# Kernel tuning notes

Measured on AMD Instinct MI355X. Metric: run time of the kernel, lower is better.

## Reference

```python
import jax, jax.numpy as jnp
import numpy as np

LN_EPS = 1e-7

def gelu(x):
    # BERT erf-based gelu
    return 0.5 * x * (1.0 + jax.lax.erf(x / jnp.sqrt(2.0).astype(x.dtype)))

def setup_inputs() -> dict:
    key = jax.random.key(0)
    k1, k2 = jax.random.split(key)
    B, S, H, I = 4, 4096, 1024, 4096
    hidden_states = jax.random.normal(k1, (B, S, H), dtype=jnp.float32)
    W = jax.random.normal(k2, (H, I), dtype=jnp.float32) * (1.0 / np.sqrt(H))
    b = jnp.zeros((I,), dtype=jnp.float32)
    ln_gamma = jnp.ones((H,), dtype=jnp.float32)
    ln_beta = jnp.zeros((H,), dtype=jnp.float32)
    return {"hidden_states": hidden_states, "ln_gamma": ln_gamma, "ln_beta": ln_beta, "W": W, "b": b}

def reference(hidden_states, ln_gamma, ln_beta, W, b):
    # LayerNorm over last dim
    mu = jnp.mean(hidden_states, axis=-1, keepdims=True)
    xc = hidden_states - mu
    var = jnp.mean(xc * xc, axis=-1, keepdims=True)
    x_norm = xc * jax.lax.rsqrt(var + LN_EPS) * ln_gamma + ln_beta
    # Linear projection [B,S,H] @ [H,I] + b, then gelu
    y = jnp.einsum('bsh,hi->bsi', x_norm, W) + b
    return gelu(y)
```

## Files before the change

kernel.cpp:

```cpp
#include <hip/hip_runtime.h>
#include <hip/hip_bf16.h>

typedef __attribute__((ext_vector_type(8))) short bf16x8;
typedef __attribute__((ext_vector_type(4))) float f32x4;

static __device__ __forceinline__ unsigned short f2bf(float f) {
    unsigned u = __builtin_bit_cast(unsigned, f);
    unsigned rounding = 0x7fffu + ((u >> 16) & 1u);
    u += rounding;
    return (unsigned short)(u >> 16);
}

static __device__ __forceinline__ void async_copy16(const void* g, void* l) {
    __builtin_amdgcn_global_load_lds(
        (const __attribute__((address_space(1))) unsigned int*)g,
        (__attribute__((address_space(3))) unsigned int*)l,
        16, 0, 0);
}

#define BARRIER() __builtin_amdgcn_s_barrier()
#define VM0()    do { asm volatile("s_waitcnt vmcnt(0)" ::: "memory"); \
                      __builtin_amdgcn_sched_barrier(0); } while (0)

static __device__ __forceinline__ float fast_gelu(float y) {
    float u = 0.7978845608028654f * y * (1.0f + 0.044715f * y * y);
    float au = fminf(fabsf(u), 9.0f);
    float e = __expf(-2.0f * au);
    float th = (1.0f - e) * __builtin_amdgcn_rcpf(1.0f + e);
    th = (u < 0.0f) ? -th : th;
    return 0.5f * y * (1.0f + th);
}

__global__ __launch_bounds__(256) void ln_cast_kernel(
    const float* __restrict__ x, const float* __restrict__ gamma,
    const float* __restrict__ beta, unsigned short* __restrict__ out) {
    const int row = blockIdx.x;
    const int t = threadIdx.x;
    const float4 v = ((const float4*)(x + (size_t)row * 1024))[t];

    float s  = v.x + v.y + v.z + v.w;
    float ss = v.x * v.x + v.y * v.y + v.z * v.z + v.w * v.w;
    #pragma unroll
    for (int off = 32; off; off >>= 1) {
        s  += __shfl_down(s, off);
        ss += __shfl_down(ss, off);
    }
    __shared__ float red[8];
    const int wid = t >> 6, lane = t & 63;
    if (lane == 0) { red[wid] = s; red[wid + 4] = ss; }
    __syncthreads();
    if (t == 0) {
        float S  = red[0] + red[1] + red[2] + red[3];
        float SS = red[4] + red[5] + red[6] + red[7];
        float mu = S * (1.0f / 1024.0f);
        float var = SS * (1.0f / 1024.0f) - mu * mu;
        red[0] = mu;
        red[1] = rsqrtf(var + 1e-7f);
    }
    __syncthreads();
    const float mu = red[0], rs = red[1];
    const float4 g = ((const float4*)gamma)[t];
    const float4 b = ((const float4*)beta)[t];

    ushort4 pk;
    pk.x = f2bf((v.x - mu) * rs * g.x + b.x);
    pk.y = f2bf((v.y - mu) * rs * g.y + b.y);
    pk.z = f2bf((v.z - mu) * rs * g.z + b.z);
    pk.w = f2bf((v.w - mu) * rs * g.w + b.w);
    ((ushort4*)(out + (size_t)row * 1024))[t] = pk;
}

__global__ __launch_bounds__(256) void wt_cast_kernel(
    const float* __restrict__ W, unsigned short* __restrict__ Wt) {
    __shared__ float tile[32][33];
    const int bx = blockIdx.x;
    const int by = blockIdx.y;
    const int tx = threadIdx.x & 31;
    const int ty = threadIdx.x >> 5;
    #pragma unroll
    for (int i = 0; i < 4; ++i) {
        int k = by * 32 + ty + i * 8;
        tile[ty + i * 8][tx] = W[(size_t)k * 4096 + bx * 32 + tx];
    }
    __syncthreads();
    #pragma unroll
    for (int i = 0; i < 4; ++i) {
        int n = bx * 32 + ty + i * 8;
        Wt[(size_t)n * 1024 + by * 32 + tx] = f2bf(tile[tx][ty + i * 8]);
    }
}

__global__ __launch_bounds__(512, 2) void gemm_kernel(
    const unsigned short* __restrict__ A, const unsigned short* __restrict__ Wt,
    const float* __restrict__ bias, float* __restrict__ out) {
    __shared__ char lds_mem[131072];

    const int bid = blockIdx.x;
    const int swz = (bid & 7) * 128 + (bid >> 3);
    const int bm = swz >> 4;
    const int bn = swz & 15;

    const int t = threadIdx.x;
    const int lane = t & 63;
    const int wid = t >> 6;
    const int wm = wid >> 2;
    const int wn = wid & 3;
    const int lrow = lane & 15;
    const int lk = lane >> 4;

    const int srr = t >> 3;
    const int sch = t & 7;
    const int sgc = sch ^ (srr & 7);
    const unsigned short* gA = A  + (size_t)(bm * 256 + srr) * 1024 + sgc * 8;
    const unsigned short* gB = Wt + (size_t)(bn * 256 + srr) * 1024 + sgc * 8;
    const int lst = srr * 128 + sch * 16;

    auto stage = [&](int kt, char* buf) {
        #pragma unroll
        for (int i = 0; i < 4; ++i) {
            async_copy16(gA + (size_t)(i * 64) * 1024 + kt * 64, buf + i * 64 * 128 + lst);
            async_copy16(gB + (size_t)(i * 64) * 1024 + kt * 64, buf + 32768 + i * 64 * 128 + lst);
        }
    };

    const int ck0 = ((lk) ^ (lrow & 7)) * 16;
    const int ck1 = ((4 + lk) ^ (lrow & 7)) * 16;
    const int aBase = (wm * 128 + lrow) * 128;
    const int bBase = 32768 + (wn * 64 + lrow) * 128;

    f32x4 acc[8][4];
    #pragma unroll
    for (int i = 0; i < 8; ++i)
        #pragma unroll
        for (int j = 0; j < 4; ++j) acc[i][j] = (f32x4)0.0f;

    float bv[4];
    #pragma unroll
    for (int ni = 0; ni < 4; ++ni) bv[ni] = bias[bn * 256 + wn * 64 + ni * 16 + lrow];

    stage(0, lds_mem);
    VM0();
    BARRIER();

    const int NKT = 16;
    for (int kt = 0; kt < NKT; ++kt) {
        char* cbuf = lds_mem + ((kt & 1) << 16);
        char* nbuf = lds_mem + (((kt + 1) & 1) << 16);

        bf16x8 bf[4][2];
        #pragma unroll
        for (int ni = 0; ni < 4; ++ni) {
            const char* p = cbuf + bBase + ni * 16 * 128;
            bf[ni][0] = *(const bf16x8*)(p + ck0);
            bf[ni][1] = *(const bf16x8*)(p + ck1);
        }

        if (kt + 1 < NKT) stage(kt + 1, nbuf);

        __builtin_amdgcn_s_setprio(1);
        #pragma unroll
        for (int mi = 0; mi < 8; ++mi) {
            const char* p = cbuf + aBase + mi * 16 * 128;
            bf16x8 a0 = *(const bf16x8*)(p + ck0);
            bf16x8 a1 = *(const bf16x8*)(p + ck1);
            #pragma unroll
            for (int ni = 0; ni < 4; ++ni) {
                acc[mi][ni] = __builtin_amdgcn_mfma_f32_16x16x32_bf16(a0, bf[ni][0], acc[mi][ni], 0, 0, 0);
                acc[mi][ni] = __builtin_amdgcn_mfma_f32_16x16x32_bf16(a1, bf[ni][1], acc[mi][ni], 0, 0, 0);
            }
        }
        __builtin_amdgcn_s_setprio(0);

        if (kt + 1 < NKT) {
            VM0();
            BARRIER();
        }
    }

    #pragma unroll
    for (int mi = 0; mi < 8; ++mi) {
        const int row0 = bm * 256 + wm * 128 + mi * 16 + lk * 4;
        #pragma unroll
        for (int ni = 0; ni < 4; ++ni) {
            const int col = bn * 256 + wn * 64 + ni * 16 + lrow;
            #pragma unroll
            for (int r = 0; r < 4; ++r) {
                float y = acc[mi][ni][r] + bv[ni];
                out[(size_t)(row0 + r) * 4096 + col] = fast_gelu(y);
            }
        }
    }
}

extern "C" void kernel_launch(void* const* d_in, const int* in_sizes, int n_in,
                              void* d_out, int out_size, void* d_ws, size_t ws_size,
                              hipStream_t stream) {
    const float* hidden = (const float*)d_in[0];
    const float* gamma  = (const float*)d_in[1];
    const float* beta   = (const float*)d_in[2];
    const float* W      = (const float*)d_in[3];
    const float* bias   = (const float*)d_in[4];
    float* out = (float*)d_out;

    unsigned short* Abf = (unsigned short*)d_ws;
    unsigned short* Wt  = (unsigned short*)((char*)d_ws + (size_t)16384 * 1024 * 2);

    ln_cast_kernel<<<16384, 256, 0, stream>>>(hidden, gamma, beta, Abf);
    wt_cast_kernel<<<dim3(128, 32), 256, 0, stream>>>(W, Wt);
    gemm_kernel<<<1024, 512, 0, stream>>>(Abf, Wt, bias, out);
}
```

Measured before the change: 184.6 us.

## Triple-buffer GEMM LDS with prefetch distance two and smaller K tile

The GEMM K-tile is halved from 64 to 32, so it now takes 32 iterations. LDS goes from two 64 KB buffers to three 32 KB buffers, with loads issued two tiles ahead and a partial vmcnt wait, so global loads are no longer fully drained before each barrier. The LDS swizzle and load mapping are rewritten for 64-byte rows. The trade-off is twice as many barriers and fewer MFMAs between them, in exchange for deeper latency hiding and a smaller LDS footprint.

```diff
diff --git a/kernel.cpp b/kernel.cpp
--- a/kernel.cpp
+++ b/kernel.cpp
@@ -19,7 +19,7 @@
 }
 
 #define BARRIER() __builtin_amdgcn_s_barrier()
-#define VM0()    do { asm volatile("s_waitcnt vmcnt(0)" ::: "memory"); \
+#define VMCNT(N) do { asm volatile("s_waitcnt vmcnt(" #N ")" ::: "memory"); \
                       __builtin_amdgcn_sched_barrier(0); } while (0)
 
 static __device__ __forceinline__ float fast_gelu(float y) {
@@ -93,7 +93,7 @@
 __global__ __launch_bounds__(512, 2) void gemm_kernel(
     const unsigned short* __restrict__ A, const unsigned short* __restrict__ Wt,
     const float* __restrict__ bias, float* __restrict__ out) {
-    __shared__ char lds_mem[131072];
+    __shared__ char lds_mem[98304];
 
     const int bid = blockIdx.x;
     const int swz = (bid & 7) * 128 + (bid >> 3);
@@ -108,25 +108,22 @@
     const int lrow = lane & 15;
     const int lk = lane >> 4;
 
-    const int srr = t >> 3;
-    const int sch = t & 7;
-    const int sgc = sch ^ (srr & 7);
+    const int srr = t >> 2;
+    const int sgc = (t & 3) ^ ((t >> 3) & 3);
     const unsigned short* gA = A  + (size_t)(bm * 256 + srr) * 1024 + sgc * 8;
     const unsigned short* gB = Wt + (size_t)(bn * 256 + srr) * 1024 + sgc * 8;
-    const int lst = srr * 128 + sch * 16;
+    const int lslot = t * 16;
 
     auto stage = [&](int kt, char* buf) {
-        #pragma unroll
-        for (int i = 0; i < 4; ++i) {
-            async_copy16(gA + (size_t)(i * 64) * 1024 + kt * 64, buf + i * 64 * 128 + lst);
-            async_copy16(gB + (size_t)(i * 64) * 1024 + kt * 64, buf + 32768 + i * 64 * 128 + lst);
-        }
+        async_copy16(gA + kt * 32,                      buf + lslot);
+        async_copy16(gA + (size_t)128 * 1024 + kt * 32, buf + 8192  + lslot);
+        async_copy16(gB + kt * 32,                      buf + 16384 + lslot);
+        async_copy16(gB + (size_t)128 * 1024 + kt * 32, buf + 24576 + lslot);
     };
 
-    const int ck0 = ((lk) ^ (lrow & 7)) * 16;
-    const int ck1 = ((4 + lk) ^ (lrow & 7)) * 16;
-    const int aBase = (wm * 128 + lrow) * 128;
-    const int bBase = 32768 + (wn * 64 + lrow) * 128;
+    const int swzc = (lk ^ ((lrow >> 1) & 3)) * 16;
+    const int aOff = (wm * 128 + lrow) * 64 + swzc;
+    const int bOff = 16384 + (wn * 64 + lrow) * 64 + swzc;
 
     f32x4 acc[8][4];
     #pragma unroll
@@ -139,42 +136,44 @@
     for (int ni = 0; ni < 4; ++ni) bv[ni] = bias[bn * 256 + wn * 64 + ni * 16 + lrow];
 
     stage(0, lds_mem);
-    VM0();
+    stage(1, lds_mem + 32768);
+    VMCNT(4);
     BARRIER();
 
-    const int NKT = 16;
+    const int NKT = 32;
+    int cb = 0;
     for (int kt = 0; kt < NKT; ++kt) {
-        char* cbuf = lds_mem + ((kt & 1) << 16);
-        char* nbuf = lds_mem + (((kt + 1) & 1) << 16);
-
-        bf16x8 bf[4][2];
-        #pragma unroll
-        for (int ni = 0; ni < 4; ++ni) {
-            const char* p = cbuf + bBase + ni * 16 * 128;
-            bf[ni][0] = *(const bf16x8*)(p + ck0);
-            bf[ni][1] = *(const bf16x8*)(p + ck1);
-        }
-
-        if (kt + 1 < NKT) stage(kt + 1, nbuf);
+        char* cbuf = lds_mem + cb * 32768;
+
+        if (kt + 2 < NKT) {
+            char* sbuf = lds_mem + ((cb >= 1) ? (cb - 1) : 2) * 32768;
+            stage(kt + 2, sbuf);
+        }
+
+        bf16x8 bf[4];
+        #pragma unroll
+        for (int ni = 0; ni < 4; ++ni)
+            bf[ni] = *(const bf16x8*)(cbuf + bOff + ni * 16 * 64);
 
         __builtin_amdgcn_s_setprio(1);
         #pragma unroll
         for (int mi = 0; mi < 8; ++mi) {
-            const char* p = cbuf + aBase + mi * 16 * 128;
-            bf16x8 a0 = *(const bf16x8*)(p + ck0);
-            bf16x8 a1 = *(const bf16x8*)(p + ck1);
+            bf16x8 a = *(const bf16x8*)(cbuf + aOff + mi * 16 * 64);
             #pragma unroll
-            for (int ni = 0; ni < 4; ++ni) {
-                acc[mi][ni] = __builtin_amdgcn_mfma_f32_16x16x32_bf16(a0, bf[ni][0], acc[mi][ni], 0, 0, 0);
-                acc[mi][ni] = __builtin_amdgcn_mfma_f32_16x16x32_bf16(a1, bf[ni][1], acc[mi][ni], 0, 0, 0);
-            }
+            for (int ni = 0; ni < 4; ++ni)
+                acc[mi][ni] = __builtin_amdgcn_mfma_f32_16x16x32_bf16(
+                    a, bf[ni], acc[mi][ni], 0, 0, 0);
         }
         __builtin_amdgcn_s_setprio(0);
 
-        if (kt + 1 < NKT) {
-            VM0();
+        if (kt < NKT - 2) {
+            VMCNT(4);
             BARRIER();
-        }
+        } else if (kt == NKT - 2) {
+            VMCNT(0);
+            BARRIER();
+        }
+        cb = (cb == 2) ? 0 : cb + 1;
     }
 
     #pragma unroll
```

Measured after the change: 193.7 us. 1.05x slower.

## Dedicate a producer wavefront to async global-to-LDS loads in GEMM

Applied to the files above, without the earlier changes.

Adds a ninth wavefront per GEMM block that issues all global-to-LDS async copies for the double-buffered A and B tiles, while the eight compute waves only read LDS and run MFMAs. The goal is to take load issue and vmcnt waits off the compute waves so MFMA work overlaps memory traffic. The trade-off is that one wave now issues 64 copies per k-step and must drain them before each barrier, which may become the bottleneck. The launch bounds also change to 576 threads with one block per CU, which changes the register budget.

```diff
diff --git a/kernel.cpp b/kernel.cpp
--- a/kernel.cpp
+++ b/kernel.cpp
@@ -90,7 +90,7 @@
     }
 }
 
-__global__ __launch_bounds__(512, 2) void gemm_kernel(
+__global__ __launch_bounds__(576, 1) void gemm_kernel(
     const unsigned short* __restrict__ A, const unsigned short* __restrict__ Wt,
     const float* __restrict__ bias, float* __restrict__ out) {
     __shared__ char lds_mem[131072];
@@ -103,26 +103,44 @@
     const int t = threadIdx.x;
     const int lane = t & 63;
     const int wid = t >> 6;
+
+    char* lds0 = lds_mem;
+    char* lds1 = lds_mem + 65536;
+    const int NKT = 16;
+
+    if (wid == 8) {
+        const int prow = lane >> 3;
+        const int pch = lane & 7;
+        const int pgc = pch ^ prow;
+        const unsigned short* pA = A  + (size_t)(bm * 256 + prow) * 1024 + pgc * 8;
+        const unsigned short* pB = Wt + (size_t)(bn * 256 + prow) * 1024 + pgc * 8;
+        const int plds = prow * 128 + pch * 16;
+
+        auto stageP = [&](int kt, char* buf) {
+            #pragma unroll
+            for (int j = 0; j < 32; ++j)
+                async_copy16(pA + (size_t)j * 8192 + kt * 64, buf + j * 1024 + plds);
+            #pragma unroll
+            for (int j = 0; j < 32; ++j)
+                async_copy16(pB + (size_t)j * 8192 + kt * 64, buf + 32768 + j * 1024 + plds);
+        };
+
+        stageP(0, lds0);
+        VM0();
+        BARRIER();
+        for (int kt = 0; kt < NKT - 1; ++kt) {
+            stageP(kt + 1, ((kt + 1) & 1) ? lds1 : lds0);
+            VM0();
+            BARRIER();
+        }
+        return;
+    }
+
     const int wm = wid >> 2;
     const int wn = wid & 3;
     const int lrow = lane & 15;
     const int lk = lane >> 4;
 
-    const int srr = t >> 3;
-    const int sch = t & 7;
-    const int sgc = sch ^ (srr & 7);
-    const unsigned short* gA = A  + (size_t)(bm * 256 + srr) * 1024 + sgc * 8;
-    const unsigned short* gB = Wt + (size_t)(bn * 256 + srr) * 1024 + sgc * 8;
-    const int lst = srr * 128 + sch * 16;
-
-    auto stage = [&](int kt, char* buf) {
-        #pragma unroll
-        for (int i = 0; i < 4; ++i) {
-            async_copy16(gA + (size_t)(i * 64) * 1024 + kt * 64, buf + i * 64 * 128 + lst);
-            async_copy16(gB + (size_t)(i * 64) * 1024 + kt * 64, buf + 32768 + i * 64 * 128 + lst);
-        }
-    };
-
     const int ck0 = ((lk) ^ (lrow & 7)) * 16;
     const int ck1 = ((4 + lk) ^ (lrow & 7)) * 16;
     const int aBase = (wm * 128 + lrow) * 128;
@@ -138,14 +156,10 @@
     #pragma unroll
     for (int ni = 0; ni < 4; ++ni) bv[ni] = bias[bn * 256 + wn * 64 + ni * 16 + lrow];
 
-    stage(0, lds_mem);
-    VM0();
     BARRIER();
 
-    const int NKT = 16;
     for (int kt = 0; kt < NKT; ++kt) {
-        char* cbuf = lds_mem + ((kt & 1) << 16);
-        char* nbuf = lds_mem + (((kt + 1) & 1) << 16);
+        char* cbuf = (kt & 1) ? lds1 : lds0;
 
         bf16x8 bf[4][2];
         #pragma unroll
@@ -155,8 +169,6 @@
             bf[ni][1] = *(const bf16x8*)(p + ck1);
         }
 
-        if (kt + 1 < NKT) stage(kt + 1, nbuf);
-
         __builtin_amdgcn_s_setprio(1);
         #pragma unroll
         for (int mi = 0; mi < 8; ++mi) {
@@ -171,10 +183,7 @@
         }
         __builtin_amdgcn_s_setprio(0);
 
-        if (kt + 1 < NKT) {
-            VM0();
-            BARRIER();
-        }
+        if (kt + 1 < NKT) BARRIER();
     }
 
     #pragma unroll
@@ -207,5 +216,5 @@
 
     ln_cast_kernel<<<16384, 256, 0, stream>>>(hidden, gamma, beta, Abf);
     wt_cast_kernel<<<dim3(128, 32), 256, 0, stream>>>(W, Wt);
-    gemm_kernel<<<1024, 512, 0, stream>>>(Abf, Wt, bias, out);
-}
+    gemm_kernel<<<1024, 576, 0, stream>>>(Abf, Wt, bias, out);
+}
```

Result: slower. 214.3 us (+16.1%).

## Make GEMM persistent with next-tile prefetch during epilogue; merge prep kernels

Applied to the files above, without the earlier changes.

The LayerNorm-cast and weight-transpose-cast kernels are merged into one launch that dispatches on block index, saving a kernel launch. The GEMM becomes persistent: 256 blocks each process 4 output tiles, and each block issues the async loads for its next tile's first K-slice before running the GELU epilogue of the current tile. This hides the epilogue and prologue latency. The cost is lower occupancy, since launch bounds drop to 1 block per CU, and less tolerance for load imbalance.

```diff
diff --git a/kernel.cpp b/kernel.cpp
--- a/kernel.cpp
+++ b/kernel.cpp
@@ -31,75 +31,72 @@
     return 0.5f * y * (1.0f + th);
 }
 
-__global__ __launch_bounds__(256) void ln_cast_kernel(
+__global__ __launch_bounds__(256) void prep_kernel(
     const float* __restrict__ x, const float* __restrict__ gamma,
-    const float* __restrict__ beta, unsigned short* __restrict__ out) {
-    const int row = blockIdx.x;
+    const float* __restrict__ beta, unsigned short* __restrict__ Aout,
+    const float* __restrict__ W, unsigned short* __restrict__ Wt) {
+    __shared__ float smem[33 * 32];
+    const int b = blockIdx.x;
     const int t = threadIdx.x;
-    const float4 v = ((const float4*)(x + (size_t)row * 1024))[t];
-
-    float s  = v.x + v.y + v.z + v.w;
-    float ss = v.x * v.x + v.y * v.y + v.z * v.z + v.w * v.w;
-    #pragma unroll
-    for (int off = 32; off; off >>= 1) {
-        s  += __shfl_down(s, off);
-        ss += __shfl_down(ss, off);
+
+    if (b < 16384) {
+        const int row = b;
+        const float4 v = ((const float4*)(x + (size_t)row * 1024))[t];
+        float s  = v.x + v.y + v.z + v.w;
+        float ss = v.x * v.x + v.y * v.y + v.z * v.z + v.w * v.w;
+        #pragma unroll
+        for (int off = 32; off; off >>= 1) {
+            s  += __shfl_down(s, off);
+            ss += __shfl_down(ss, off);
+        }
+        const int wid = t >> 6, lane = t & 63;
+        if (lane == 0) { smem[wid] = s; smem[wid + 4] = ss; }
+        __syncthreads();
+        if (t == 0) {
+            float S  = smem[0] + smem[1] + smem[2] + smem[3];
+            float SS = smem[4] + smem[5] + smem[6] + smem[7];
+            float mu = S * (1.0f / 1024.0f);
+            float var = SS * (1.0f / 1024.0f) - mu * mu;
+            smem[0] = mu;
+            smem[1] = rsqrtf(var + 1e-7f);
+        }
+        __syncthreads();
+        const float mu = smem[0], rs = smem[1];
+        const float4 g = ((const float4*)gamma)[t];
+        const float4 be = ((const float4*)beta)[t];
+        ushort4 pk;
+        pk.x = f2bf((v.x - mu) * rs * g.x + be.x);
+        pk.y = f2bf((v.y - mu) * rs * g.y + be.y);
+        pk.z = f2bf((v.z - mu) * rs * g.z + be.z);
+        pk.w = f2bf((v.w - mu) * rs * g.w + be.w);
+        ((ushort4*)(Aout + (size_t)row * 1024))[t] = pk;
+    } else {
+        const int r = b - 16384;
+        const int bx = r & 127;
+        const int by = r >> 7;
+        float (*tile)[33] = (float(*)[33])smem;
+        const int tx = t & 31;
+        const int ty = t >> 5;
+        #pragma unroll
+        for (int i = 0; i < 4; ++i) {
+            int k = by * 32 + ty + i * 8;
+            tile[ty + i * 8][tx] = W[(size_t)k * 4096 + bx * 32 + tx];
+        }
+        __syncthreads();
+        #pragma unroll
+        for (int i = 0; i < 4; ++i) {
+            int n = bx * 32 + ty + i * 8;
+            Wt[(size_t)n * 1024 + by * 32 + tx] = f2bf(tile[tx][ty + i * 8]);
+        }
     }
-    __shared__ float red[8];
-    const int wid = t >> 6, lane = t & 63;
-    if (lane == 0) { red[wid] = s; red[wid + 4] = ss; }
-    __syncthreads();
-    if (t == 0) {
-        float S  = red[0] + red[1] + red[2] + red[3];
-        float SS = red[4] + red[5] + red[6] + red[7];
-        float mu = S * (1.0f / 1024.0f);
-        float var = SS * (1.0f / 1024.0f) - mu * mu;
-        red[0] = mu;
-        red[1] = rsqrtf(var + 1e-7f);
-    }
-    __syncthreads();
-    const float mu = red[0], rs = red[1];
-    const float4 g = ((const float4*)gamma)[t];
-    const float4 b = ((const float4*)beta)[t];
-
-    ushort4 pk;
-    pk.x = f2bf((v.x - mu) * rs * g.x + b.x);
-    pk.y = f2bf((v.y - mu) * rs * g.y + b.y);
-    pk.z = f2bf((v.z - mu) * rs * g.z + b.z);
-    pk.w = f2bf((v.w - mu) * rs * g.w + b.w);
-    ((ushort4*)(out + (size_t)row * 1024))[t] = pk;
-}
-
-__global__ __launch_bounds__(256) void wt_cast_kernel(
-    const float* __restrict__ W, unsigned short* __restrict__ Wt) {
-    __shared__ float tile[32][33];
-    const int bx = blockIdx.x;
-    const int by = blockIdx.y;
-    const int tx = threadIdx.x & 31;
-    const int ty = threadIdx.x >> 5;
-    #pragma unroll
-    for (int i = 0; i < 4; ++i) {
-        int k = by * 32 + ty + i * 8;
-        tile[ty + i * 8][tx] = W[(size_t)k * 4096 + bx * 32 + tx];
-    }
-    __syncthreads();
-    #pragma unroll
-    for (int i = 0; i < 4; ++i) {
-        int n = bx * 32 + ty + i * 8;
-        Wt[(size_t)n * 1024 + by * 32 + tx] = f2bf(tile[tx][ty + i * 8]);
-    }
-}
-
-__global__ __launch_bounds__(512, 2) void gemm_kernel(
+}
+
+__global__ __launch_bounds__(512, 1) void gemm_kernel(
     const unsigned short* __restrict__ A, const unsigned short* __restrict__ Wt,
     const float* __restrict__ bias, float* __restrict__ out) {
     __shared__ char lds_mem[131072];
 
     const int bid = blockIdx.x;
-    const int swz = (bid & 7) * 128 + (bid >> 3);
-    const int bm = swz >> 4;
-    const int bn = swz & 15;
-
     const int t = threadIdx.x;
     const int lane = t & 63;
     const int wid = t >> 6;
@@ -111,83 +108,111 @@
     const int srr = t >> 3;
     const int sch = t & 7;
     const int sgc = sch ^ (srr & 7);
-    const unsigned short* gA = A  + (size_t)(bm * 256 + srr) * 1024 + sgc * 8;
-    const unsigned short* gB = Wt + (size_t)(bn * 256 + srr) * 1024 + sgc * 8;
     const int lst = srr * 128 + sch * 16;
-
-    auto stage = [&](int kt, char* buf) {
-        #pragma unroll
-        for (int i = 0; i < 4; ++i) {
-            async_copy16(gA + (size_t)(i * 64) * 1024 + kt * 64, buf + i * 64 * 128 + lst);
-            async_copy16(gB + (size_t)(i * 64) * 1024 + kt * 64, buf + 32768 + i * 64 * 128 + lst);
-        }
-    };
 
     const int ck0 = ((lk) ^ (lrow & 7)) * 16;
     const int ck1 = ((4 + lk) ^ (lrow & 7)) * 16;
     const int aBase = (wm * 128 + lrow) * 128;
     const int bBase = 32768 + (wn * 64 + lrow) * 128;
 
-    f32x4 acc[8][4];
-    #pragma unroll
-    for (int i = 0; i < 8; ++i)
-        #pragma unroll
-        for (int j = 0; j < 4; ++j) acc[i][j] = (f32x4)0.0f;
-
-    float bv[4];
-    #pragma unroll
-    for (int ni = 0; ni < 4; ++ni) bv[ni] = bias[bn * 256 + wn * 64 + ni * 16 + lrow];
-
-    stage(0, lds_mem);
+    char* lds0 = lds_mem;
+    char* lds1 = lds_mem + 65536;
+
+    auto tileBase = [&](int tau, const unsigned short*& gA, const unsigned short*& gB,
+                        int& bm, int& bn) {
+        const int swz = (tau & 7) * 128 + (tau >> 3);
+        bm = swz >> 4;
+        bn = swz & 15;
+        gA = A  + (size_t)(bm * 256 + srr) * 1024 + sgc * 8;
+        gB = Wt + (size_t)(bn * 256 + srr) * 1024 + sgc * 8;
+    };
+
+    auto stage = [&](const unsigned short* gA, const unsigned short* gB,
+                     int kt, char* buf) {
+        #pragma unroll
+        for (int i = 0; i < 4; ++i) {
+            async_copy16(gA + (size_t)(i * 64) * 1024 + kt * 64, buf + i * 64 * 128 + lst);
+            async_copy16(gB + (size_t)(i * 64) * 1024 + kt * 64, buf + 32768 + i * 64 * 128 + lst);
+        }
+    };
+
+    const unsigned short *gA, *gB;
+    int bm, bn;
+    tileBase(bid, gA, gB, bm, bn);
+    stage(gA, gB, 0, lds0);
     VM0();
     BARRIER();
 
     const int NKT = 16;
-    for (int kt = 0; kt < NKT; ++kt) {
-        char* cbuf = lds_mem + ((kt & 1) << 16);
-        char* nbuf = lds_mem + (((kt + 1) & 1) << 16);
-
-        bf16x8 bf[4][2];
-        #pragma unroll
-        for (int ni = 0; ni < 4; ++ni) {
-            const char* p = cbuf + bBase + ni * 16 * 128;
-            bf[ni][0] = *(const bf16x8*)(p + ck0);
-            bf[ni][1] = *(const bf16x8*)(p + ck1);
-        }
-
-        if (kt + 1 < NKT) stage(kt + 1, nbuf);
-
-        __builtin_amdgcn_s_setprio(1);
+    for (int i = 0; i < 4; ++i) {
+        f32x4 acc[8][4];
+        #pragma unroll
+        for (int a = 0; a < 8; ++a)
+            #pragma unroll
+            for (int j = 0; j < 4; ++j) acc[a][j] = (f32x4)0.0f;
+
+        float bv[4];
+        #pragma unroll
+        for (int ni = 0; ni < 4; ++ni) bv[ni] = bias[bn * 256 + wn * 64 + ni * 16 + lrow];
+
+        for (int kt = 0; kt < NKT; ++kt) {
+            char* cbuf = (kt & 1) ? lds1 : lds0;
+            char* nbuf = (kt & 1) ? lds0 : lds1;
+
+            bf16x8 bf[4][2];
+            #pragma unroll
+            for (int ni = 0; ni < 4; ++ni) {
+                const char* p = cbuf + bBase + ni * 16 * 128;
+                bf[ni][0] = *(const bf16x8*)(p + ck0);
+                bf[ni][1] = *(const bf16x8*)(p + ck1);
+            }
+
+            if (kt + 1 < NKT) stage(gA, gB, kt + 1, nbuf);
+
+            __builtin_amdgcn_s_setprio(1);
+            #pragma unroll
+            for (int mi = 0; mi < 8; ++mi) {
+                const char* p = cbuf + aBase + mi * 16 * 128;
+                bf16x8 a0 = *(const bf16x8*)(p + ck0);
+                bf16x8 a1 = *(const bf16x8*)(p + ck1);
+                #pragma unroll
+                for (int ni = 0; ni < 4; ++ni) {
+                    acc[mi][ni] = __builtin_amdgcn_mfma_f32_16x16x32_bf16(a0, bf[ni][0], acc[mi][ni], 0, 0, 0);
+                    acc[mi][ni] = __builtin_amdgcn_mfma_f32_16x16x32_bf16(a1, bf[ni][1], acc[mi][ni], 0, 0, 0);
+                }
+            }
+            __builtin_amdgcn_s_setprio(0);
+
+            if (kt + 1 < NKT) {
+                VM0();
+                BARRIER();
+            }
+        }
+
+        const int row0base = bm * 256 + wm * 128;
+        const int colbase  = bn * 256 + wn * 64;
+        if (i + 1 < 4) {
+            tileBase(bid + 256 * (i + 1), gA, gB, bm, bn);
+            stage(gA, gB, 0, lds0);
+        }
+
         #pragma unroll
         for (int mi = 0; mi < 8; ++mi) {
-            const char* p = cbuf + aBase + mi * 16 * 128;
-            bf16x8 a0 = *(const bf16x8*)(p + ck0);
-            bf16x8 a1 = *(const bf16x8*)(p + ck1);
+            const int row0 = row0base + mi * 16 + lk * 4;
             #pragma unroll
             for (int ni = 0; ni < 4; ++ni) {
-                acc[mi][ni] = __builtin_amdgcn_mfma_f32_16x16x32_bf16(a0, bf[ni][0], acc[mi][ni], 0, 0, 0);
-                acc[mi][ni] = __builtin_amdgcn_mfma_f32_16x16x32_bf16(a1, bf[ni][1], acc[mi][ni], 0, 0, 0);
-            }
-        }
-        __builtin_amdgcn_s_setprio(0);
-
-        if (kt + 1 < NKT) {
+                const int col = colbase + ni * 16 + lrow;
+                #pragma unroll
+                for (int r = 0; r < 4; ++r) {
+                    float y = acc[mi][ni][r] + bv[ni];
+                    out[(size_t)(row0 + r) * 4096 + col] = fast_gelu(y);
+                }
+            }
+        }
+
+        if (i + 1 < 4) {
             VM0();
             BARRIER();
-        }
-    }
-
-    #pragma unroll
-    for (int mi = 0; mi < 8; ++mi) {
-        const int row0 = bm * 256 + wm * 128 + mi * 16 + lk * 4;
-        #pragma unroll
-        for (int ni = 0; ni < 4; ++ni) {
-            const int col = bn * 256 + wn * 64 + ni * 16 + lrow;
-            #pragma unroll
-            for (int r = 0; r < 4; ++r) {
-                float y = acc[mi][ni][r] + bv[ni];
-                out[(size_t)(row0 + r) * 4096 + col] = fast_gelu(y);
-            }
         }
     }
 }
@@ -205,7 +230,6 @@
     unsigned short* Abf = (unsigned short*)d_ws;
     unsigned short* Wt  = (unsigned short*)((char*)d_ws + (size_t)16384 * 1024 * 2);
 
-    ln_cast_kernel<<<16384, 256, 0, stream>>>(hidden, gamma, beta, Abf);
-    wt_cast_kernel<<<dim3(128, 32), 256, 0, stream>>>(W, Wt);
-    gemm_kernel<<<1024, 512, 0, stream>>>(Abf, Wt, bias, out);
-}
+    prep_kernel<<<16384 + 4096, 256, 0, stream>>>(hidden, gamma, beta, Abf, W, Wt);
+    gemm_kernel<<<256, 512, 0, stream>>>(Abf, Wt, bias, out);
+}
```

Measured after the change: 182.8 us. No clear change (-1.0%).
